# Kernel tuning notes

Measured on AMD Instinct MI355X. Metric: run time of the kernel, lower is better.

The kernel has to match this reference:

```python
import jax, jax.numpy as jnp
import numpy as np

B, S, D = 2, 4096, 512
H = 8
HD = D // H  # head dim = 64
NEG = -9e15


def setup_inputs() -> dict:
    key = jax.random.key(0)
    ks = jax.random.split(key, 6)
    x = jax.random.normal(ks[0], (B, S, D), dtype=jnp.float32)
    mask = jax.random.randint(ks[1], (B, S), 0, 2, dtype=jnp.int32)
    # Linear params, torch default init scale ~ 1/sqrt(fan_in)
    w_qkv = jax.random.normal(ks[2], (D, 3 * D), dtype=jnp.float32) / np.sqrt(D)
    b_qkv = jax.random.normal(ks[3], (3 * D,), dtype=jnp.float32) * 0.01
    w_o = jax.random.normal(ks[4], (D, D), dtype=jnp.float32) / np.sqrt(D)
    b_o = jax.random.normal(ks[5], (D,), dtype=jnp.float32) * 0.01
    return {"x": x, "mask": mask, "w_qkv": w_qkv, "b_qkv": b_qkv, "w_o": w_o, "b_o": b_o}


def reference(x, mask, w_qkv, b_qkv, w_o, b_o):
    b, s, d = x.shape
    qkv = x @ w_qkv + b_qkv                      # [B,S,3D]
    qkv = qkv.reshape(b, s, H, 3 * HD).transpose(0, 2, 1, 3)  # [B,H,S,3*HD]
    q, k, v = jnp.split(qkv, 3, axis=-1)         # each [B,H,S,HD]
    logits = jnp.einsum('bhqd,bhkd->bhqk', q, k) / np.sqrt(HD)
    m = mask[:, None, None, :]                   # [B,1,1,S]
    logits = jnp.where(m == 0, NEG, logits)
    attention = jax.nn.softmax(logits, axis=-1)  # [B,H,S,S]
    values = jnp.einsum('bhqk,bhkd->bhqd', attention, v)
    values = values.transpose(0, 2, 1, 3).reshape(b, s, d)
    o = values @ w_o + b_o
    return o, attention
```

## Files before the change

### kernel.cpp

```cpp
#include <hip/hip_runtime.h>
#include <math.h>

#define BB   2
#define SS   4096
#define DD   512
#define HH   8
#define HDIM 64

typedef short s16x8 __attribute__((ext_vector_type(8)));
typedef float f32x4 __attribute__((ext_vector_type(4)));

__device__ __forceinline__ unsigned short f2bf(float f) {
    union { float f; unsigned int u; } cv; cv.f = f;
    const unsigned int u = cv.u;
    return (unsigned short)((u + 0x7fffu + ((u >> 16) & 1u)) >> 16);
}

__global__ __launch_bounds__(256)
void qkv_gemm(const float* __restrict__ x, const float* __restrict__ w,
              const float* __restrict__ bias,
              unsigned short* __restrict__ Qb, unsigned short* __restrict__ Kb,
              unsigned short* __restrict__ Vtb)
{
    __shared__ float As[64][20];
    __shared__ float Bs[16][64];
    const int tid = threadIdx.x;
    const int ty = tid >> 4, tx = tid & 15;
    const int m0 = blockIdx.x * 64;
    const int n0 = blockIdx.y * 64;
    const int N  = 3 * DD;

    float c[4][4] = {};

    for (int k0 = 0; k0 < DD; k0 += 16) {
        {
            const int r  = tid >> 2;
            const int c4 = (tid & 3) * 4;
            *(float4*)&As[r][c4] =
                *(const float4*)&x[(size_t)(m0 + r) * DD + k0 + c4];
            const int br  = tid >> 4;
            const int bc4 = (tid & 15) * 4;
            *(float4*)&Bs[br][bc4] =
                *(const float4*)&w[(size_t)(k0 + br) * N + n0 + bc4];
        }
        __syncthreads();
        #pragma unroll
        for (int kk0 = 0; kk0 < 16; kk0 += 4) {
            float4 a4[4];
            #pragma unroll
            for (int i = 0; i < 4; ++i) a4[i] = *(const float4*)&As[ty + 16*i][kk0];
            #pragma unroll
            for (int w4 = 0; w4 < 4; ++w4) {
                float bv[4];
                #pragma unroll
                for (int j = 0; j < 4; ++j) bv[j] = Bs[kk0 + w4][tx + 16*j];
                #pragma unroll
                for (int i = 0; i < 4; ++i) {
                    const float av = ((const float*)&a4[i])[w4];
                    #pragma unroll
                    for (int j = 0; j < 4; ++j) c[i][j] = fmaf(av, bv[j], c[i][j]);
                }
            }
        }
        __syncthreads();
    }

    const int h    = n0 / 192;
    const int kind = (n0 % 192) / 64;
    #pragma unroll
    for (int i = 0; i < 4; ++i) {
        const int t  = m0 + ty + 16*i;
        const int bb = t >> 12;
        const int s  = t & 4095;
        const int bh = bb * HH + h;
        #pragma unroll
        for (int j = 0; j < 4; ++j) {
            const int d = tx + 16*j;
            const unsigned short bf = f2bf(c[i][j] + bias[n0 + d]);
            if (kind == 2)
                Vtb[((size_t)bh * HDIM + d) * SS + s] = bf;
            else if (kind == 1)
                Kb[((size_t)bh * SS + s) * HDIM + d] = bf;
            else
                Qb[((size_t)bh * SS + s) * HDIM + d] = bf;
        }
    }
}

__global__ __launch_bounds__(256)
void attn_fused(const unsigned short* __restrict__ Qb,
                const unsigned short* __restrict__ Kb,
                const unsigned short* __restrict__ Vtb,
                const int* __restrict__ mask,
                float* __restrict__ attn, float* __restrict__ val)
{
    __shared__ unsigned short Ps[4][16][72];
    const int tid  = threadIdx.x;
    const int wave = tid >> 6;
    const int lane = tid & 63;
    const int lgrp = lane >> 4;
    const int lcol = lane & 15;
    const int q0   = blockIdx.x * 64;
    const int bh   = blockIdx.y;
    const int b    = bh >> 3;

    const unsigned short* Qh  = Qb  + (size_t)bh * SS * HDIM;
    const unsigned short* Kh  = Kb  + (size_t)bh * SS * HDIM;
    const unsigned short* Vth = Vtb + (size_t)bh * HDIM * SS;
    float* attn_bh = attn + (size_t)bh * SS * SS;
    const int* mrow = mask + b * SS;

    const int qrow = q0 + wave * 16 + lcol;
    s16x8 qf[2];
    qf[0] = *(const s16x8*)&Qh[(size_t)qrow * HDIM +      lgrp * 8];
    qf[1] = *(const s16x8*)&Qh[(size_t)qrow * HDIM + 32 + lgrp * 8];

    float m_r[4], l_r[4];
    #pragma unroll
    for (int r = 0; r < 4; ++r) { m_r[r] = -INFINITY; l_r[r] = 0.f; }

    for (int kt = 0; kt < 64; ++kt) {
        const int k0 = kt * 64;
        s16x8 kf[4][2];
        #pragma unroll
        for (int nk = 0; nk < 4; ++nk) {
            const size_t krow = (size_t)(k0 + nk * 16 + lcol) * HDIM;
            kf[nk][0] = *(const s16x8*)&Kh[krow +      lgrp * 8];
            kf[nk][1] = *(const s16x8*)&Kh[krow + 32 + lgrp * 8];
        }
        float bias[4];
        #pragma unroll
        for (int nk = 0; nk < 4; ++nk)
            bias[nk] = mrow[k0 + nk * 16 + lcol] ? 0.f : -1e9f;

        float sv[4][4];
        #pragma unroll
        for (int nk = 0; nk < 4; ++nk) {
            f32x4 S = {0.f, 0.f, 0.f, 0.f};
            S = __builtin_amdgcn_mfma_f32_16x16x32_bf16(qf[0], kf[nk][0], S, 0, 0, 0);
            S = __builtin_amdgcn_mfma_f32_16x16x32_bf16(qf[1], kf[nk][1], S, 0, 0, 0);
            #pragma unroll
            for (int r = 0; r < 4; ++r) sv[nk][r] = S[r] * 0.125f + bias[nk];
        }
        #pragma unroll
        for (int r = 0; r < 4; ++r) {
            float tm = fmaxf(fmaxf(sv[0][r], sv[1][r]), fmaxf(sv[2][r], sv[3][r]));
            #pragma unroll
            for (int o = 1; o < 16; o <<= 1) tm = fmaxf(tm, __shfl_xor(tm, o));
            const float nm = fmaxf(m_r[r], tm);
            float se = __expf(sv[0][r] - nm) + __expf(sv[1][r] - nm)
                     + __expf(sv[2][r] - nm) + __expf(sv[3][r] - nm);
            #pragma unroll
            for (int o = 1; o < 16; o <<= 1) se += __shfl_xor(se, o);
            l_r[r] = l_r[r] * __expf(m_r[r] - nm) + se;
            m_r[r] = nm;
        }
    }
    float linv[4];
    #pragma unroll
    for (int r = 0; r < 4; ++r) linv[r] = 1.f / l_r[r];

    f32x4 acc[4];
    #pragma unroll
    for (int nd = 0; nd < 4; ++nd) acc[nd] = (f32x4){0.f, 0.f, 0.f, 0.f};

    for (int kt = 0; kt < 64; ++kt) {
        const int k0 = kt * 64;
        s16x8 kf[4][2];
        #pragma unroll
        for (int nk = 0; nk < 4; ++nk) {
            const size_t krow = (size_t)(k0 + nk * 16 + lcol) * HDIM;
            kf[nk][0] = *(const s16x8*)&Kh[krow +      lgrp * 8];
            kf[nk][1] = *(const s16x8*)&Kh[krow + 32 + lgrp * 8];
        }
        float bias[4];
        #pragma unroll
        for (int nk = 0; nk < 4; ++nk)
            bias[nk] = mrow[k0 + nk * 16 + lcol] ? 0.f : -1e9f;

        float p[4][4];
        #pragma unroll
        for (int nk = 0; nk < 4; ++nk) {
            f32x4 S = {0.f, 0.f, 0.f, 0.f};
            S = __builtin_amdgcn_mfma_f32_16x16x32_bf16(qf[0], kf[nk][0], S, 0, 0, 0);
            S = __builtin_amdgcn_mfma_f32_16x16x32_bf16(qf[1], kf[nk][1], S, 0, 0, 0);
            #pragma unroll
            for (int r = 0; r < 4; ++r) {
                const float sv = S[r] * 0.125f + bias[nk];
                p[nk][r] = __expf(sv - m_r[r]) * linv[r];
                Ps[wave][lgrp * 4 + r][nk * 16 + lcol] = f2bf(p[nk][r]);
            }
        }
        __syncthreads();

        #pragma unroll
        for (int nk = 0; nk < 4; ++nk)
            #pragma unroll
            for (int r = 0; r < 4; ++r)
                attn_bh[(size_t)(q0 + wave * 16 + lgrp * 4 + r) * SS
                        + k0 + nk * 16 + lcol] = p[nk][r];

        s16x8 pa[2];
        pa[0] = *(const s16x8*)&Ps[wave][lcol][     lgrp * 8];
        pa[1] = *(const s16x8*)&Ps[wave][lcol][32 + lgrp * 8];

        s16x8 vf[4][2];
        #pragma unroll
        for (int nd = 0; nd < 4; ++nd) {
            const size_t vrow = (size_t)(nd * 16 + lcol) * SS + k0;
            vf[nd][0] = *(const s16x8*)&Vth[vrow +      lgrp * 8];
            vf[nd][1] = *(const s16x8*)&Vth[vrow + 32 + lgrp * 8];
        }
        #pragma unroll
        for (int nd = 0; nd < 4; ++nd) {
            acc[nd] = __builtin_amdgcn_mfma_f32_16x16x32_bf16(pa[0], vf[nd][0], acc[nd], 0, 0, 0);
            acc[nd] = __builtin_amdgcn_mfma_f32_16x16x32_bf16(pa[1], vf[nd][1], acc[nd], 0, 0, 0);
        }
    }

    #pragma unroll
    for (int nd = 0; nd < 4; ++nd)
        #pragma unroll
        for (int r = 0; r < 4; ++r)
            val[((size_t)bh * SS + q0 + wave * 16 + lgrp * 4 + r) * HDIM
                + nd * 16 + lcol] = acc[nd][r];
}

__global__ __launch_bounds__(256)
void oproj_gemm(const float* __restrict__ val, const float* __restrict__ w,
                const float* __restrict__ bias, float* __restrict__ out)
{
    __shared__ float As[64][20];
    __shared__ float Bs[16][64];
    const int tid = threadIdx.x;
    const int ty = tid >> 4, tx = tid & 15;
    const int m0 = blockIdx.x * 64;
    const int n0 = blockIdx.y * 64;

    float c[4][4] = {};

    for (int k0 = 0; k0 < DD; k0 += 16) {
        {
            const int r   = tid >> 2;
            const int c4  = (tid & 3) * 4;
            const int t   = m0 + r;
            const int bb  = t >> 12;
            const int s   = t & 4095;
            const int head = k0 >> 6;
            const int d    = (k0 & 63) + c4;
            *(float4*)&As[r][c4] =
                *(const float4*)&val[(((size_t)bb * HH + head) * SS + s) * HDIM + d];
            const int br  = tid >> 4;
            const int bc4 = (tid & 15) * 4;
            *(float4*)&Bs[br][bc4] =
                *(const float4*)&w[(size_t)(k0 + br) * DD + n0 + bc4];
        }
        __syncthreads();
        #pragma unroll
        for (int kk0 = 0; kk0 < 16; kk0 += 4) {
            float4 a4[4];
            #pragma unroll
            for (int i = 0; i < 4; ++i) a4[i] = *(const float4*)&As[ty + 16*i][kk0];
            #pragma unroll
            for (int w4 = 0; w4 < 4; ++w4) {
                float bv[4];
                #pragma unroll
                for (int j = 0; j < 4; ++j) bv[j] = Bs[kk0 + w4][tx + 16*j];
                #pragma unroll
                for (int i = 0; i < 4; ++i) {
                    const float av = ((const float*)&a4[i])[w4];
                    #pragma unroll
                    for (int j = 0; j < 4; ++j) c[i][j] = fmaf(av, bv[j], c[i][j]);
                }
            }
        }
        __syncthreads();
    }
    #pragma unroll
    for (int i = 0; i < 4; ++i) {
        const int t = m0 + ty + 16*i;
        #pragma unroll
        for (int j = 0; j < 4; ++j) {
            const int n = n0 + tx + 16*j;
            out[(size_t)t * DD + n] = c[i][j] + bias[n];
        }
    }
}

extern "C" void kernel_launch(void* const* d_in, const int* in_sizes, int n_in,
                              void* d_out, int out_size, void* d_ws, size_t ws_size,
                              hipStream_t stream)
{
    const float* x     = (const float*)d_in[0];
    const int*   mask  = (const int*)d_in[1];
    const float* w_qkv = (const float*)d_in[2];
    const float* b_qkv = (const float*)d_in[3];
    const float* w_o   = (const float*)d_in[4];
    const float* b_o   = (const float*)d_in[5];

    float* out  = (float*)d_out;
    float* attn = out + (size_t)BB * SS * DD;

    const size_t nqkv = (size_t)BB * HH * SS * HDIM;
    unsigned short* Qb  = (unsigned short*)d_ws;
    unsigned short* Kb  = Qb + nqkv;
    unsigned short* Vtb = Kb + nqkv;
    float*          val = (float*)(Vtb + nqkv);

    qkv_gemm  <<<dim3(128, 24), 256, 0, stream>>>(x, w_qkv, b_qkv, Qb, Kb, Vtb);
    attn_fused<<<dim3(64, 16),  256, 0, stream>>>(Qb, Kb, Vtb, mask, attn, val);
    oproj_gemm<<<dim3(128, 8),  256, 0, stream>>>(val, w_o, b_o, out);
}
```

Baseline: 1.996 ms.

## Vectorize QKV stores, transpose QK MFMA, stage fp32 P in LDS for coalesced attn writes

New measurement: 3.142 ms. 57.4% more time.

```diff
diff --git a/kernel.cpp b/kernel.cpp
--- a/kernel.cpp
+++ b/kernel.cpp
@@ -10,10 +10,21 @@
 typedef short s16x8 __attribute__((ext_vector_type(8)));
 typedef float f32x4 __attribute__((ext_vector_type(4)));
 
+struct alignas(8) us4 { unsigned short x, y, z, w; };
+
 __device__ __forceinline__ unsigned short f2bf(float f) {
     union { float f; unsigned int u; } cv; cv.f = f;
     const unsigned int u = cv.u;
     return (unsigned short)((u + 0x7fffu + ((u >> 16) & 1u)) >> 16);
+}
+
+__device__ __forceinline__ s16x8 pack_bf8(float4 a, float4 b) {
+    union { s16x8 v; unsigned int u[4]; } r;
+    r.u[0] = (unsigned)f2bf(a.x) | ((unsigned)f2bf(a.y) << 16);
+    r.u[1] = (unsigned)f2bf(a.z) | ((unsigned)f2bf(a.w) << 16);
+    r.u[2] = (unsigned)f2bf(b.x) | ((unsigned)f2bf(b.y) << 16);
+    r.u[3] = (unsigned)f2bf(b.z) | ((unsigned)f2bf(b.w) << 16);
+    return r.v;
 }
 
 __global__ __launch_bounds__(256)
@@ -48,17 +59,17 @@
         for (int kk0 = 0; kk0 < 16; kk0 += 4) {
             float4 a4[4];
             #pragma unroll
-            for (int i = 0; i < 4; ++i) a4[i] = *(const float4*)&As[ty + 16*i][kk0];
+            for (int i = 0; i < 4; ++i) a4[i] = *(const float4*)&As[ty * 4 + i][kk0];
             #pragma unroll
             for (int w4 = 0; w4 < 4; ++w4) {
-                float bv[4];
-                #pragma unroll
-                for (int j = 0; j < 4; ++j) bv[j] = Bs[kk0 + w4][tx + 16*j];
+                const float4 bv = *(const float4*)&Bs[kk0 + w4][tx * 4];
                 #pragma unroll
                 for (int i = 0; i < 4; ++i) {
                     const float av = ((const float*)&a4[i])[w4];
-                    #pragma unroll
-                    for (int j = 0; j < 4; ++j) c[i][j] = fmaf(av, bv[j], c[i][j]);
+                    c[i][0] = fmaf(av, bv.x, c[i][0]);
+                    c[i][1] = fmaf(av, bv.y, c[i][1]);
+                    c[i][2] = fmaf(av, bv.z, c[i][2]);
+                    c[i][3] = fmaf(av, bv.w, c[i][3]);
                 }
             }
         }
@@ -67,22 +78,36 @@
 
     const int h    = n0 / 192;
     const int kind = (n0 % 192) / 64;
-    #pragma unroll
-    for (int i = 0; i < 4; ++i) {
-        const int t  = m0 + ty + 16*i;
-        const int bb = t >> 12;
-        const int s  = t & 4095;
+    if (kind != 2) {
+        unsigned short* dst = kind ? Kb : Qb;
+        #pragma unroll
+        for (int i = 0; i < 4; ++i) {
+            const int t  = m0 + ty * 4 + i;
+            const int bb = t >> 12;
+            const int s  = t & 4095;
+            const int bh = bb * HH + h;
+            us4 o;
+            o.x = f2bf(c[i][0] + bias[n0 + tx * 4 + 0]);
+            o.y = f2bf(c[i][1] + bias[n0 + tx * 4 + 1]);
+            o.z = f2bf(c[i][2] + bias[n0 + tx * 4 + 2]);
+            o.w = f2bf(c[i][3] + bias[n0 + tx * 4 + 3]);
+            *(us4*)&dst[((size_t)bh * SS + s) * HDIM + tx * 4] = o;
+        }
+    } else {
+        const int t0 = m0 + ty * 4;
+        const int bb = t0 >> 12;
+        const int s0 = t0 & 4095;
         const int bh = bb * HH + h;
         #pragma unroll
         for (int j = 0; j < 4; ++j) {
-            const int d = tx + 16*j;
-            const unsigned short bf = f2bf(c[i][j] + bias[n0 + d]);
-            if (kind == 2)
-                Vtb[((size_t)bh * HDIM + d) * SS + s] = bf;
-            else if (kind == 1)
-                Kb[((size_t)bh * SS + s) * HDIM + d] = bf;
-            else
-                Qb[((size_t)bh * SS + s) * HDIM + d] = bf;
+            const int d = tx * 4 + j;
+            const float bz = bias[n0 + d];
+            us4 o;
+            o.x = f2bf(c[0][j] + bz);
+            o.y = f2bf(c[1][j] + bz);
+            o.z = f2bf(c[2][j] + bz);
+            o.w = f2bf(c[3][j] + bz);
+            *(us4*)&Vtb[((size_t)bh * HDIM + d) * SS + s0] = o;
         }
     }
 }
@@ -94,7 +119,8 @@
                 const int* __restrict__ mask,
                 float* __restrict__ attn, float* __restrict__ val)
 {
-    __shared__ unsigned short Ps[4][16][72];
+    __shared__ unsigned int Mb[SS / 4];
+    __shared__ float Pf[4][16][68];
     const int tid  = threadIdx.x;
     const int wave = tid >> 6;
     const int lane = tid & 63;
@@ -110,111 +136,103 @@
     float* attn_bh = attn + (size_t)bh * SS * SS;
     const int* mrow = mask + b * SS;
 
+    for (int t = tid; t < SS / 4; t += 256) {
+        const int4 mv = *(const int4*)&mrow[t * 4];
+        Mb[t] = (unsigned)(mv.x & 1) | ((unsigned)(mv.y & 1) << 8)
+              | ((unsigned)(mv.z & 1) << 16) | ((unsigned)(mv.w & 1) << 24);
+    }
+    __syncthreads();
+
     const int qrow = q0 + wave * 16 + lcol;
-    s16x8 qf[2];
-    qf[0] = *(const s16x8*)&Qh[(size_t)qrow * HDIM +      lgrp * 8];
-    qf[1] = *(const s16x8*)&Qh[(size_t)qrow * HDIM + 32 + lgrp * 8];
-
-    float m_r[4], l_r[4];
-    #pragma unroll
-    for (int r = 0; r < 4; ++r) { m_r[r] = -INFINITY; l_r[r] = 0.f; }
+    const s16x8 qf0 = *(const s16x8*)&Qh[(size_t)qrow * HDIM +      lgrp * 8];
+    const s16x8 qf1 = *(const s16x8*)&Qh[(size_t)qrow * HDIM + 32 + lgrp * 8];
+
+    float m_ln = -INFINITY, l_ln = 0.f;
 
     for (int kt = 0; kt < 64; ++kt) {
         const int k0 = kt * 64;
-        s16x8 kf[4][2];
+        float sv[16];
         #pragma unroll
         for (int nk = 0; nk < 4; ++nk) {
             const size_t krow = (size_t)(k0 + nk * 16 + lcol) * HDIM;
-            kf[nk][0] = *(const s16x8*)&Kh[krow +      lgrp * 8];
-            kf[nk][1] = *(const s16x8*)&Kh[krow + 32 + lgrp * 8];
-        }
-        float bias[4];
-        #pragma unroll
-        for (int nk = 0; nk < 4; ++nk)
-            bias[nk] = mrow[k0 + nk * 16 + lcol] ? 0.f : -1e9f;
-
-        float sv[4][4];
-        #pragma unroll
-        for (int nk = 0; nk < 4; ++nk) {
+            const s16x8 kf0 = *(const s16x8*)&Kh[krow +      lgrp * 8];
+            const s16x8 kf1 = *(const s16x8*)&Kh[krow + 32 + lgrp * 8];
             f32x4 S = {0.f, 0.f, 0.f, 0.f};
-            S = __builtin_amdgcn_mfma_f32_16x16x32_bf16(qf[0], kf[nk][0], S, 0, 0, 0);
-            S = __builtin_amdgcn_mfma_f32_16x16x32_bf16(qf[1], kf[nk][1], S, 0, 0, 0);
-            #pragma unroll
-            for (int r = 0; r < 4; ++r) sv[nk][r] = S[r] * 0.125f + bias[nk];
-        }
-        #pragma unroll
-        for (int r = 0; r < 4; ++r) {
-            float tm = fmaxf(fmaxf(sv[0][r], sv[1][r]), fmaxf(sv[2][r], sv[3][r]));
-            #pragma unroll
-            for (int o = 1; o < 16; o <<= 1) tm = fmaxf(tm, __shfl_xor(tm, o));
-            const float nm = fmaxf(m_r[r], tm);
-            float se = __expf(sv[0][r] - nm) + __expf(sv[1][r] - nm)
-                     + __expf(sv[2][r] - nm) + __expf(sv[3][r] - nm);
-            #pragma unroll
-            for (int o = 1; o < 16; o <<= 1) se += __shfl_xor(se, o);
-            l_r[r] = l_r[r] * __expf(m_r[r] - nm) + se;
-            m_r[r] = nm;
-        }
-    }
-    float linv[4];
-    #pragma unroll
-    for (int r = 0; r < 4; ++r) linv[r] = 1.f / l_r[r];
+            S = __builtin_amdgcn_mfma_f32_16x16x32_bf16(kf0, qf0, S, 0, 0, 0);
+            S = __builtin_amdgcn_mfma_f32_16x16x32_bf16(kf1, qf1, S, 0, 0, 0);
+            const unsigned mw = Mb[kt * 16 + nk * 4 + lgrp];
+            #pragma unroll
+            for (int r = 0; r < 4; ++r)
+                sv[nk * 4 + r] = ((mw >> (8 * r)) & 0xffu) ? S[r] * 0.125f : -1e9f;
+        }
+        float mx[8];
+        #pragma unroll
+        for (int i = 0; i < 8; ++i) mx[i] = fmaxf(sv[i], sv[i + 8]);
+        #pragma unroll
+        for (int i = 0; i < 4; ++i) mx[i] = fmaxf(mx[i], mx[i + 4]);
+        float tm = fmaxf(fmaxf(mx[0], mx[1]), fmaxf(mx[2], mx[3]));
+        tm = fmaxf(tm, __shfl_xor(tm, 16));
+        tm = fmaxf(tm, __shfl_xor(tm, 32));
+        const float nm = fmaxf(m_ln, tm);
+        #pragma unroll
+        for (int i = 0; i < 16; ++i) sv[i] = __expf(sv[i] - nm);
+        #pragma unroll
+        for (int i = 0; i < 8; ++i) sv[i] += sv[i + 8];
+        #pragma unroll
+        for (int i = 0; i < 4; ++i) sv[i] += sv[i + 4];
+        float se = (sv[0] + sv[1]) + (sv[2] + sv[3]);
+        se += __shfl_xor(se, 16);
+        se += __shfl_xor(se, 32);
+        l_ln = l_ln * __expf(m_ln - nm) + se;
+        m_ln = nm;
+    }
+    const float linv = (l_ln > 0.f) ? 1.f / l_ln : 0.f;
 
     f32x4 acc[4];
     #pragma unroll
     for (int nd = 0; nd < 4; ++nd) acc[nd] = (f32x4){0.f, 0.f, 0.f, 0.f};
 
+    float (*Pw)[68] = Pf[wave];
+    const int prow = lane >> 2;
+    const int pcol = (lane & 3) * 16;
+
     for (int kt = 0; kt < 64; ++kt) {
         const int k0 = kt * 64;
-        s16x8 kf[4][2];
         #pragma unroll
         for (int nk = 0; nk < 4; ++nk) {
             const size_t krow = (size_t)(k0 + nk * 16 + lcol) * HDIM;
-            kf[nk][0] = *(const s16x8*)&Kh[krow +      lgrp * 8];
-            kf[nk][1] = *(const s16x8*)&Kh[krow + 32 + lgrp * 8];
-        }
-        float bias[4];
-        #pragma unroll
-        for (int nk = 0; nk < 4; ++nk)
-            bias[nk] = mrow[k0 + nk * 16 + lcol] ? 0.f : -1e9f;
-
-        float p[4][4];
-        #pragma unroll
-        for (int nk = 0; nk < 4; ++nk) {
+            const s16x8 kf0 = *(const s16x8*)&Kh[krow +      lgrp * 8];
+            const s16x8 kf1 = *(const s16x8*)&Kh[krow + 32 + lgrp * 8];
             f32x4 S = {0.f, 0.f, 0.f, 0.f};
-            S = __builtin_amdgcn_mfma_f32_16x16x32_bf16(qf[0], kf[nk][0], S, 0, 0, 0);
-            S = __builtin_amdgcn_mfma_f32_16x16x32_bf16(qf[1], kf[nk][1], S, 0, 0, 0);
-            #pragma unroll
-            for (int r = 0; r < 4; ++r) {
-                const float sv = S[r] * 0.125f + bias[nk];
-                p[nk][r] = __expf(sv - m_r[r]) * linv[r];
-                Ps[wave][lgrp * 4 + r][nk * 16 + lcol] = f2bf(p[nk][r]);
-            }
-        }
-        __syncthreads();
-
-        #pragma unroll
-        for (int nk = 0; nk < 4; ++nk)
-            #pragma unroll
-            for (int r = 0; r < 4; ++r)
-                attn_bh[(size_t)(q0 + wave * 16 + lgrp * 4 + r) * SS
-                        + k0 + nk * 16 + lcol] = p[nk][r];
-
-        s16x8 pa[2];
-        pa[0] = *(const s16x8*)&Ps[wave][lcol][     lgrp * 8];
-        pa[1] = *(const s16x8*)&Ps[wave][lcol][32 + lgrp * 8];
-
-        s16x8 vf[4][2];
+            S = __builtin_amdgcn_mfma_f32_16x16x32_bf16(kf0, qf0, S, 0, 0, 0);
+            S = __builtin_amdgcn_mfma_f32_16x16x32_bf16(kf1, qf1, S, 0, 0, 0);
+            const unsigned mw = Mb[kt * 16 + nk * 4 + lgrp];
+            f32x4 pq;
+            pq[0] = ( mw        & 0xffu) ? __expf(S[0] * 0.125f - m_ln) * linv : 0.f;
+            pq[1] = ((mw >>  8) & 0xffu) ? __expf(S[1] * 0.125f - m_ln) * linv : 0.f;
+            pq[2] = ((mw >> 16) & 0xffu) ? __expf(S[2] * 0.125f - m_ln) * linv : 0.f;
+            pq[3] = ((mw >> 24) & 0xffu) ? __expf(S[3] * 0.125f - m_ln) * linv : 0.f;
+            *(f32x4*)&Pw[lcol][nk * 16 + lgrp * 4] = pq;
+        }
+        const float4 pa00 = *(const float4*)&Pw[lcol][     lgrp * 8];
+        const float4 pa01 = *(const float4*)&Pw[lcol][     lgrp * 8 + 4];
+        const float4 pa10 = *(const float4*)&Pw[lcol][32 + lgrp * 8];
+        const float4 pa11 = *(const float4*)&Pw[lcol][32 + lgrp * 8 + 4];
+        const s16x8 pa0 = pack_bf8(pa00, pa01);
+        const s16x8 pa1 = pack_bf8(pa10, pa11);
         #pragma unroll
         for (int nd = 0; nd < 4; ++nd) {
             const size_t vrow = (size_t)(nd * 16 + lcol) * SS + k0;
-            vf[nd][0] = *(const s16x8*)&Vth[vrow +      lgrp * 8];
-            vf[nd][1] = *(const s16x8*)&Vth[vrow + 32 + lgrp * 8];
-        }
-        #pragma unroll
-        for (int nd = 0; nd < 4; ++nd) {
-            acc[nd] = __builtin_amdgcn_mfma_f32_16x16x32_bf16(pa[0], vf[nd][0], acc[nd], 0, 0, 0);
-            acc[nd] = __builtin_amdgcn_mfma_f32_16x16x32_bf16(pa[1], vf[nd][1], acc[nd], 0, 0, 0);
+            const s16x8 vf0 = *(const s16x8*)&Vth[vrow +      lgrp * 8];
+            const s16x8 vf1 = *(const s16x8*)&Vth[vrow + 32 + lgrp * 8];
+            acc[nd] = __builtin_amdgcn_mfma_f32_16x16x32_bf16(pa0, vf0, acc[nd], 0, 0, 0);
+            acc[nd] = __builtin_amdgcn_mfma_f32_16x16x32_bf16(pa1, vf1, acc[nd], 0, 0, 0);
+        }
+        float* gdst = &attn_bh[(size_t)(q0 + wave * 16 + prow) * SS + k0 + pcol];
+        #pragma unroll
+        for (int u = 0; u < 4; ++u) {
+            const f32x4 pv = *(const f32x4*)&Pw[prow][pcol + u * 4];
+            __builtin_nontemporal_store(pv, (f32x4*)(gdst + u * 4));
         }
     }
 
```
